# Kernel tuning notes

Measured on AMD Instinct MI355X. Metric: run time of the kernel, lower is better.

Reference implementation:

```python
import jax, jax.numpy as jnp
import numpy as np

B, C, H, W = 32, 512, 64, 64
P = 8            # partition (window) size
HEAD_DIM = 32
N_HEADS = C // HEAD_DIM  # 16
MLP_RATIO = 4
LN_EPS = 1e-5


def _rel_pos_index(p):
    # Swin/MaxViT-style relative position index for a p x p window -> [p*p, p*p]
    coords = np.stack(np.meshgrid(np.arange(p), np.arange(p), indexing='ij'), 0).reshape(2, -1)
    rel = coords[:, :, None] - coords[:, None, :]          # [2, pp, pp]
    rel = rel.transpose(1, 2, 0) + (p - 1)                 # shift to >= 0
    idx = rel[..., 0] * (2 * p - 1) + rel[..., 1]          # [pp, pp]
    return jnp.asarray(idx, jnp.int32)


def setup_inputs() -> dict:
    key = jax.random.key(0)
    ks = jax.random.split(key, 10)
    s = 0.02
    d_ff = MLP_RATIO * C
    inp = {
        'x': jax.random.normal(ks[0], (B, C, H, W), jnp.float32),
        'gamma1': jnp.ones((C,), jnp.float32),
        'beta1': jnp.zeros((C,), jnp.float32),
        'gamma2': jnp.ones((C,), jnp.float32),
        'beta2': jnp.zeros((C,), jnp.float32),
        'qkv_w': jax.random.normal(ks[1], (C, 3 * C), jnp.float32) * s,
        'qkv_b': jnp.zeros((3 * C,), jnp.float32),
        'merge_w': jax.random.normal(ks[2], (C, C), jnp.float32) * s,
        'merge_b': jnp.zeros((C,), jnp.float32),
        'bias_table': jax.random.normal(ks[3], ((2 * P - 1) ** 2, N_HEADS), jnp.float32) * s,
        'w1': jax.random.normal(ks[4], (C, d_ff), jnp.float32) * s,
        'b1': jnp.zeros((d_ff,), jnp.float32),
        'w2': jax.random.normal(ks[5], (d_ff, C), jnp.float32) * s,
        'b2': jnp.zeros((C,), jnp.float32),
        'rel_idx': _rel_pos_index(P),
    }
    return inp


def _layernorm(t, g, b):
    mu = jnp.mean(t, axis=-1, keepdims=True)
    var = jnp.mean(jnp.square(t - mu), axis=-1, keepdims=True)
    return (t - mu) * jax.lax.rsqrt(var + LN_EPS) * g + b


def reference(x, gamma1, beta1, gamma2, beta2, qkv_w, qkv_b, merge_w, merge_b,
              bias_table, w1, b1, w2, b2, rel_idx):
    p, hd, nh = P, HEAD_DIM, N_HEADS
    Bx, Cx, Hx, Wx = x.shape
    hp, wp = Hx // p, Wx // p
    G, PP = hp * wp, p * p

    # --- window partition: [B,C,H,W] -> [B, G, p*p, C] (partition_type='window', no swap)
    xw = x.reshape(Bx, Cx, hp, p, wp, p).transpose(0, 2, 4, 3, 5, 1).reshape(Bx, G, PP, Cx)

    # --- relative-position multi-head attention on norm1(x)
    h = _layernorm(xw, gamma1, beta1)
    qkv = h @ qkv_w + qkv_b                                   # [B,G,PP,3C]
    q, k, v = jnp.split(qkv, 3, axis=-1)
    q = q.reshape(Bx, G, PP, nh, hd) * (hd ** -0.5)
    k = k.reshape(Bx, G, PP, nh, hd)
    v = v.reshape(Bx, G, PP, nh, hd)
    attn = jnp.einsum('bgqhd,bgkhd->bghqk', q, k)             # [B,G,nh,PP,PP]
    bias = bias_table[rel_idx]                                # [PP,PP,nh]
    attn = attn + bias.transpose(2, 0, 1)[None, None]
    attn = jax.nn.softmax(attn, axis=-1)
    o = jnp.einsum('bghqk,bgkhd->bgqhd', attn, v).reshape(Bx, G, PP, Cx)
    xw = xw + (o @ merge_w + merge_b)                          # residual (dropout/SD p=0)

    # --- MLP block on norm2(x)
    h2 = _layernorm(xw, gamma2, beta2)
    m = jax.nn.gelu(h2 @ w1 + b1) @ w2 + b2
    xw = xw + m

    # --- window departition: [B,G,p*p,C] -> [B,C,H,W]
    out = xw.reshape(Bx, hp, wp, p, p, Cx).transpose(0, 5, 1, 3, 2, 4).reshape(Bx, Cx, Hx, Wx)
    return out
```

## Files before the change

### kernel.cpp

```cpp
#include <hip/hip_runtime.h>
#include <stdint.h>

typedef __attribute__((ext_vector_type(8))) short short8;
typedef __attribute__((ext_vector_type(4))) float f32x4;
typedef __attribute__((address_space(3))) void lds_void;
typedef __attribute__((address_space(1))) void gv_void;

static __device__ __forceinline__ float bf2f(unsigned short u) {
    union { uint32_t i; float f; } v; v.i = ((uint32_t)u) << 16; return v.f;
}
static __device__ __forceinline__ unsigned short f2bf(float f) {
    union { float f; uint32_t i; } v; v.f = f;
    uint32_t i = v.i;
    uint32_t r = (i + 0x7fffu + ((i >> 16) & 1u)) >> 16;
    return (unsigned short)r;
}
static __device__ __forceinline__ float fexp(float x) {
    float r;
    asm("v_exp_f32 %0, %1" : "=v"(r) : "v"(x * 1.44269504088896f));
    return r;
}
static __device__ __forceinline__ float frcp(float x) {
    float r;
    asm("v_rcp_f32 %0, %1" : "=v"(r) : "v"(x));
    return r;
}

__global__ void k_detect(const void* __restrict__ g1, int* __restrict__ flag) {
    if (threadIdx.x == 0 && blockIdx.x == 0) {
        const unsigned short* u = (const unsigned short*)g1;
        flag[0] = (u[0] == 0x3F80u) ? 0 : 1;
    }
}

__global__ __launch_bounds__(256) void k_cvt(const void* __restrict__ src,
                                             unsigned short* __restrict__ dst,
                                             int n, const int* __restrict__ flag) {
    int i = blockIdx.x * 256 + threadIdx.x;
    if (i < n) {
        dst[i] = flag[0] ? f2bf(((const float*)src)[i])
                         : ((const unsigned short*)src)[i];
    }
}

__global__ __launch_bounds__(256) void k_transpose(const void* __restrict__ in,
                                                   unsigned short* __restrict__ out,
                                                   int R, int C, const int* __restrict__ flag) {
    __shared__ unsigned short tile[32][33];
    int isf = flag[0];
    int tx = threadIdx.x, ty = threadIdx.y;
    int x = blockIdx.x * 32 + tx;
    int y0 = blockIdx.y * 32;
    for (int j = ty; j < 32; j += 8) {
        size_t idx = (size_t)(y0 + j) * C + x;
        tile[j][tx] = isf ? f2bf(((const float*)in)[idx]) : ((const unsigned short*)in)[idx];
    }
    __syncthreads();
    int x2 = y0 + tx;
    int y20 = blockIdx.x * 32;
    for (int j = ty; j < 32; j += 8)
        out[(size_t)(y20 + j) * R + x2] = tile[tx][j];
}

__global__ __launch_bounds__(256) void k_prep_bias(const void* __restrict__ bias_table,
                                                   const int* __restrict__ rel_idx,
                                                   float* __restrict__ biasp,
                                                   const int* __restrict__ flag) {
    int i = blockIdx.x * 256 + threadIdx.x;
    int isf = flag[0];
    int h = i & 15, qk = i >> 4;
    size_t idx = (size_t)rel_idx[qk] * 16 + h;
    float v = isf ? ((const float*)bias_table)[idx] : bf2f(((const unsigned short*)bias_table)[idx]);
    biasp[h * 4096 + qk] = v;
}

__global__ __launch_bounds__(256) void k_partition_ln(const void* __restrict__ x,
                                                      const unsigned short* __restrict__ g1,
                                                      const unsigned short* __restrict__ b1,
                                                      unsigned short* __restrict__ xw,
                                                      unsigned short* __restrict__ h,
                                                      int b0, const int* __restrict__ flag) {
    __shared__ unsigned short tile[64][512];
    int isf = flag[0];
    int bh = blockIdx.x, bl = bh >> 6, hh = bh & 63;
    int b = b0 + bl;
    int tid = threadIdx.x;
    size_t xoff = (((size_t)b * 512) * 64 + hh) * 64;
    int c0 = tid >> 3, ch = tid & 7;
    if (isf) {
        const float* xb = (const float*)x + xoff;
        for (int k = 0; k < 16; ++k) {
            int c = c0 + k * 32;
            f32x4 v0 = *reinterpret_cast<const f32x4*>(xb + (size_t)c * 4096 + ch * 8);
            f32x4 v1 = *reinterpret_cast<const f32x4*>(xb + (size_t)c * 4096 + ch * 8 + 4);
#pragma unroll
            for (int j = 0; j < 4; ++j) tile[ch * 8 + j][c] = f2bf(v0[j]);
#pragma unroll
            for (int j = 0; j < 4; ++j) tile[ch * 8 + 4 + j][c] = f2bf(v1[j]);
        }
    } else {
        const unsigned short* xb = (const unsigned short*)x + xoff;
        for (int k = 0; k < 16; ++k) {
            int c = c0 + k * 32;
            short8 v = *reinterpret_cast<const short8*>(xb + (size_t)c * 4096 + ch * 8);
#pragma unroll
            for (int j = 0; j < 8; ++j) tile[ch * 8 + j][c] = (unsigned short)v[j];
        }
    }
    __syncthreads();
    int w = tid >> 2, q = tid & 3;
    float s = 0.f, s2 = 0.f;
#pragma unroll 4
    for (int j = 0; j < 128; ++j) {
        int c = q * 128 + ((j + 8 * w) & 127);
        float f = bf2f(tile[w][c]);
        s += f; s2 += f * f;
    }
    s += __shfl_xor(s, 1);  s += __shfl_xor(s, 2);
    s2 += __shfl_xor(s2, 1); s2 += __shfl_xor(s2, 2);
    float mu = s * (1.f / 512.f);
    float rstd = rsqrtf(s2 * (1.f / 512.f) - mu * mu + 1e-5f);
    int t = (bl * 64 + (hh >> 3) * 8 + (w >> 3)) * 64 + (hh & 7) * 8 + (w & 7);
    unsigned short* xr = xw + (size_t)t * 512;
    unsigned short* hr = h + (size_t)t * 512;
    for (int cc = q * 128; cc < q * 128 + 128; cc += 8) {
        short8 raw, hn;
#pragma unroll
        for (int j = 0; j < 8; ++j) {
            unsigned short u = tile[w][cc + j];
            raw[j] = (short)u;
            float f = (bf2f(u) - mu) * rstd * bf2f(g1[cc + j]) + bf2f(b1[cc + j]);
            hn[j] = (short)f2bf(f);
        }
        *reinterpret_cast<short8*>(xr + cc) = raw;
        *reinterpret_cast<short8*>(hr + cc) = hn;
    }
}

__global__ __launch_bounds__(256) void k_ln(const unsigned short* __restrict__ in,
                                            const unsigned short* __restrict__ g,
                                            const unsigned short* __restrict__ b,
                                            unsigned short* __restrict__ out) {
    int wid = threadIdx.x >> 6, lane = threadIdx.x & 63;
    size_t t = (size_t)blockIdx.x * 4 + wid;
    short8 v = *reinterpret_cast<const short8*>(in + t * 512 + lane * 8);
    float f[8], s = 0.f, s2 = 0.f;
#pragma unroll
    for (int j = 0; j < 8; ++j) { f[j] = bf2f((unsigned short)v[j]); s += f[j]; s2 += f[j] * f[j]; }
    for (int m = 1; m < 64; m <<= 1) { s += __shfl_xor(s, m); s2 += __shfl_xor(s2, m); }
    float mu = s * (1.f / 512.f);
    float rstd = rsqrtf(s2 * (1.f / 512.f) - mu * mu + 1e-5f);
    short8 ov;
#pragma unroll
    for (int j = 0; j < 8; ++j)
        ov[j] = (short)f2bf((f[j] - mu) * rstd * bf2f(g[lane * 8 + j]) + bf2f(b[lane * 8 + j]));
    *reinterpret_cast<short8*>(out + t * 512 + lane * 8) = ov;
}

template <int MODE>
__global__ __launch_bounds__(512, 2) void k_gemm3(const unsigned short* __restrict__ A,
                                                  const unsigned short* __restrict__ BT,
                                                  const unsigned short* __restrict__ bias,
                                                  const unsigned short* __restrict__ res,
                                                  unsigned short* __restrict__ out,
                                                  int M, int N, int K) {
    __shared__ unsigned short S[65536];
    const int tid = threadIdx.x, lane = tid & 63, wid = tid >> 6;
    const int mt = blockIdx.x, nt = blockIdx.y;
    const int wr = wid >> 2, wc = wid & 3;
    const int rl = lane & 15, qg = lane >> 4;

    const unsigned short* ApA[2];
    const unsigned short* ApB[2];
#pragma unroll
    for (int h = 0; h < 2; ++h) {
        int row = h * 128 + wid * 16 + (lane >> 2);
        int blk = (lane & 3) ^ ((row >> 1) & 3);
        ApA[h] = A  + (size_t)(mt * 256 + row) * K + blk * 8;
        ApB[h] = BT + (size_t)(nt * 256 + row) * K + blk * 8;
    }

    f32x4 acc[8][4];
#pragma unroll
    for (int mf = 0; mf < 8; ++mf)
#pragma unroll
        for (int nf = 0; nf < 4; ++nf) {
            acc[mf][nf][0] = 0.f; acc[mf][nf][1] = 0.f; acc[mf][nf][2] = 0.f; acc[mf][nf][3] = 0.f;
        }

    const int NT = K >> 5;

    auto stage = [&](int t, int h) {
        int slot = t & 3;
        __builtin_amdgcn_global_load_lds((const gv_void*)(ApA[h] + t * 32),
            (lds_void*)(&S[slot * 16384 + h * 4096 + wid * 512]), 16, 0, 0);
        __builtin_amdgcn_global_load_lds((const gv_void*)(ApB[h] + t * 32),
            (lds_void*)(&S[slot * 16384 + 8192 + h * 4096 + wid * 512]), 16, 0, 0);
    };

    stage(0, 0); stage(0, 1);
    stage(1, 0); stage(1, 1);
    stage(2, 0); stage(2, 1);

    const int xo = ((qg ^ ((rl >> 1) & 3))) * 8;
    const int arow = wr * 128 + rl;
    const int brow = wc * 64 + rl;

    for (int t = 0; t < NT; ++t) {
        const unsigned short* sA = &S[(t & 3) * 16384];
        const unsigned short* sB = sA + 8192;
        if (t + 3 < NT) stage(t + 3, 0);
        if (t + 3 < NT)      { asm volatile("s_waitcnt vmcnt(10)" ::: "memory"); }
        else if (t + 2 < NT) { asm volatile("s_waitcnt vmcnt(8)"  ::: "memory"); }
        else if (t + 1 < NT) { asm volatile("s_waitcnt vmcnt(4)"  ::: "memory"); }
        else                 { asm volatile("s_waitcnt vmcnt(0)"  ::: "memory"); }
        __builtin_amdgcn_s_barrier();
        asm volatile("" ::: "memory");

        short8 bfr[4], af[4];
#pragma unroll
        for (int nf = 0; nf < 4; ++nf)
            bfr[nf] = *reinterpret_cast<const short8*>(&sB[(brow + nf * 16) * 32 + xo]);
#pragma unroll
        for (int mf = 0; mf < 4; ++mf)
            af[mf] = *reinterpret_cast<const short8*>(&sA[(arow + mf * 16) * 32 + xo]);
        if (t + 3 < NT) stage(t + 3, 1);

        __builtin_amdgcn_s_setprio(1);
#pragma unroll
        for (int mf = 0; mf < 4; ++mf)
#pragma unroll
            for (int nf = 0; nf < 4; ++nf)
                acc[mf][nf] = __builtin_amdgcn_mfma_f32_16x16x32_bf16(af[mf], bfr[nf], acc[mf][nf], 0, 0, 0);
        __builtin_amdgcn_s_setprio(0);

        short8 af2[4];
#pragma unroll
        for (int mf = 0; mf < 4; ++mf)
            af2[mf] = *reinterpret_cast<const short8*>(&sA[(arow + 64 + mf * 16) * 32 + xo]);
        __builtin_amdgcn_s_barrier();
        asm volatile("" ::: "memory");
        __builtin_amdgcn_s_setprio(1);
#pragma unroll
        for (int mf = 0; mf < 4; ++mf)
#pragma unroll
            for (int nf = 0; nf < 4; ++nf)
                acc[mf + 4][nf] = __builtin_amdgcn_mfma_f32_16x16x32_bf16(af2[mf], bfr[nf], acc[mf + 4][nf], 0, 0, 0);
        __builtin_amdgcn_s_setprio(0);
        __builtin_amdgcn_s_barrier();
        asm volatile("" ::: "memory");
    }

    const int PST = 272;
    unsigned short* pb = (unsigned short*)S;
    float bz[4];
#pragma unroll
    for (int nf = 0; nf < 4; ++nf) bz[nf] = bf2f(bias[nt * 256 + wc * 64 + nf * 16 + rl]);
    int row_l = tid >> 4, cbl = (tid & 15) * 16;
    int growb = mt * 256 + (row_l >> 4) * 128 + (row_l & 15);
    size_t gcol = (size_t)nt * 256 + cbl;

#pragma unroll
    for (int mf = 0; mf < 8; ++mf) {
        __syncthreads();
#pragma unroll
        for (int nf = 0; nf < 4; ++nf)
#pragma unroll
            for (int r = 0; r < 4; ++r) {
                float v = acc[mf][nf][r] + bz[nf];
                if (MODE == 2) {
                    float z = 0.7978845608f * (v + 0.044715f * v * v * v);
                    float e = fexp(-2.0f * z);
                    v = v * frcp(1.f + e);
                }
                pb[(wr * 16 + qg * 4 + r) * PST + wc * 64 + nf * 16 + rl] = f2bf(v);
            }
        __syncthreads();
        size_t go = (size_t)(growb + mf * 16) * N + gcol;
        short8 o1 = *reinterpret_cast<const short8*>(&pb[row_l * PST + cbl]);
        short8 o2 = *reinterpret_cast<const short8*>(&pb[row_l * PST + cbl + 8]);
        if (MODE == 1) {
            short8 r1 = *reinterpret_cast<const short8*>(&res[go]);
            short8 r2 = *reinterpret_cast<const short8*>(&res[go + 8]);
#pragma unroll
            for (int j = 0; j < 8; ++j) {
                o1[j] = (short)f2bf(bf2f((unsigned short)o1[j]) + bf2f((unsigned short)r1[j]));
                o2[j] = (short)f2bf(bf2f((unsigned short)o2[j]) + bf2f((unsigned short)r2[j]));
            }
        }
        *reinterpret_cast<short8*>(&out[go]) = o1;
        *reinterpret_cast<short8*>(&out[go + 8]) = o2;
    }
}

__global__ __launch_bounds__(64) void k_attn(const unsigned short* __restrict__ qkv,
                                             const float* __restrict__ biasp,
                                             unsigned short* __restrict__ o) {
    __shared__ unsigned short Pl[64][72];
    int blk = blockIdx.x;
    int head = blk & 15, win = blk >> 4;
    size_t T0 = (size_t)win * 64;
    int lane = threadIdx.x;
    int rl = lane & 15, qg = lane >> 4;
    const unsigned short* base = qkv + T0 * 1536;
    int qoff = head * 32, koff = 512 + head * 32, voff = 1024 + head * 32;

    f32x4 s[4][4];
#pragma unroll
    for (int m = 0; m < 4; ++m)
#pragma unroll
        for (int n = 0; n < 4; ++n) { s[m][n][0] = 0.f; s[m][n][1] = 0.f; s[m][n][2] = 0.f; s[m][n][3] = 0.f; }

    short8 aq[4], bk[4];
#pragma unroll
    for (int m = 0; m < 4; ++m)
        aq[m] = *reinterpret_cast<const short8*>(base + (size_t)(16 * m + rl) * 1536 + qoff + qg * 8);
#pragma unroll
    for (int n = 0; n < 4; ++n)
        bk[n] = *reinterpret_cast<const short8*>(base + (size_t)(16 * n + rl) * 1536 + koff + qg * 8);
#pragma unroll
    for (int m = 0; m < 4; ++m)
#pragma unroll
        for (int n = 0; n < 4; ++n)
            s[m][n] = __builtin_amdgcn_mfma_f32_16x16x32_bf16(aq[m], bk[n], s[m][n], 0, 0, 0);

    const float scale = 0.17677669529663687f;
    const float* bh = biasp + head * 4096;
#pragma unroll
    for (int m = 0; m < 4; ++m) {
#pragma unroll
        for (int r = 0; r < 4; ++r) {
            int row = 16 * m + qg * 4 + r;
            float v0 = s[m][0][r] * scale + bh[row * 64 + rl];
            float v1 = s[m][1][r] * scale + bh[row * 64 + 16 + rl];
            float v2 = s[m][2][r] * scale + bh[row * 64 + 32 + rl];
            float v3 = s[m][3][r] * scale + bh[row * 64 + 48 + rl];
            float mx = fmaxf(fmaxf(v0, v1), fmaxf(v2, v3));
            mx = fmaxf(mx, __shfl_xor(mx, 1));
            mx = fmaxf(mx, __shfl_xor(mx, 2));
            mx = fmaxf(mx, __shfl_xor(mx, 4));
            mx = fmaxf(mx, __shfl_xor(mx, 8));
            v0 = fexp(v0 - mx); v1 = fexp(v1 - mx); v2 = fexp(v2 - mx); v3 = fexp(v3 - mx);
            float sm = v0 + v1 + v2 + v3;
            sm += __shfl_xor(sm, 1);
            sm += __shfl_xor(sm, 2);
            sm += __shfl_xor(sm, 4);
            sm += __shfl_xor(sm, 8);
            float inv = frcp(sm);
            Pl[row][rl]      = f2bf(v0 * inv);
            Pl[row][16 + rl] = f2bf(v1 * inv);
            Pl[row][32 + rl] = f2bf(v2 * inv);
            Pl[row][48 + rl] = f2bf(v3 * inv);
        }
    }
    __syncthreads();

    short8 bv[2][2];
#pragma unroll
    for (int ks = 0; ks < 2; ++ks)
#pragma unroll
        for (int n2 = 0; n2 < 2; ++n2) {
            short8 t;
#pragma unroll
            for (int i = 0; i < 8; ++i)
                t[i] = (short)base[(size_t)(32 * ks + qg * 8 + i) * 1536 + voff + n2 * 16 + rl];
            bv[ks][n2] = t;
        }

    f32x4 acc2[4][2];
#pragma unroll
    for (int m = 0; m < 4; ++m)
#pragma unroll
        for (int n2 = 0; n2 < 2; ++n2) { acc2[m][n2][0] = 0.f; acc2[m][n2][1] = 0.f; acc2[m][n2][2] = 0.f; acc2[m][n2][3] = 0.f; }

#pragma unroll
    for (int m = 0; m < 4; ++m) {
        short8 p0 = *reinterpret_cast<const short8*>(&Pl[16 * m + rl][qg * 8]);
        short8 p1 = *reinterpret_cast<const short8*>(&Pl[16 * m + rl][32 + qg * 8]);
#pragma unroll
        for (int n2 = 0; n2 < 2; ++n2) {
            acc2[m][n2] = __builtin_amdgcn_mfma_f32_16x16x32_bf16(p0, bv[0][n2], acc2[m][n2], 0, 0, 0);
            acc2[m][n2] = __builtin_amdgcn_mfma_f32_16x16x32_bf16(p1, bv[1][n2], acc2[m][n2], 0, 0, 0);
        }
    }
#pragma unroll
    for (int m = 0; m < 4; ++m)
#pragma unroll
        for (int n2 = 0; n2 < 2; ++n2)
#pragma unroll
            for (int r = 0; r < 4; ++r) {
                int row = 16 * m + qg * 4 + r;
                o[(T0 + row) * 512 + head * 32 + n2 * 16 + rl] = f2bf(acc2[m][n2][r]);
            }
}

__global__ __launch_bounds__(256) void k_departition(const unsigned short* __restrict__ tok,
                                                     void* __restrict__ xo,
                                                     int b0, const int* __restrict__ flag) {
    __shared__ unsigned short tile[64][512];
    int isf = flag[0];
    int bh = blockIdx.x, bl = bh >> 6, hh = bh & 63;
    int b = b0 + bl;
    int tid = threadIdx.x;
    int Tb = (bl * 64 + (hh >> 3) * 8) * 64 + (hh & 7) * 8;
    for (int k = 0; k < 16; ++k) {
        int flat = k * 256 + tid;
        int w = flat >> 6, ch = flat & 63;
        int t = Tb + (w >> 3) * 64 + (w & 7);
        short8 v = *reinterpret_cast<const short8*>(tok + (size_t)t * 512 + ch * 8);
        *reinterpret_cast<short8*>(&tile[w][ch * 8]) = v;
    }
    __syncthreads();
    size_t xoff = (((size_t)b * 512) * 64 + hh) * 64;
    if (isf) {
        float* xb = (float*)xo + xoff;
        for (int k = 0; k < 16; ++k) {
            int flat = k * 256 + tid;
            int c = flat >> 3, wc = flat & 7;
#pragma unroll
            for (int j = 0; j < 8; ++j)
                xb[(size_t)c * 4096 + wc * 8 + j] = bf2f(tile[wc * 8 + j][c]);
        }
    } else {
        unsigned short* xb = (unsigned short*)xo + xoff;
        for (int k = 0; k < 16; ++k) {
            int flat = k * 256 + tid;
            int c = flat >> 3, wc = flat & 7;
            short8 v;
#pragma unroll
            for (int j = 0; j < 8; ++j) v[j] = (short)tile[wc * 8 + j][c];
            *reinterpret_cast<short8*>(xb + (size_t)c * 4096 + wc * 8) = v;
        }
    }
}

extern "C" void kernel_launch(void* const* d_in, const int* in_sizes, int n_in,
                              void* d_out, int out_size, void* d_ws, size_t ws_size,
                              hipStream_t stream) {
    const void* x          = d_in[0];
    const void* g1         = d_in[1];
    const void* be1        = d_in[2];
    const void* g2         = d_in[3];
    const void* be2        = d_in[4];
    const void* qkv_w      = d_in[5];
    const void* qkv_b      = d_in[6];
    const void* merge_w    = d_in[7];
    const void* merge_b    = d_in[8];
    const void* bias_table = d_in[9];
    const void* w1         = d_in[10];
    const void* b1         = d_in[11];
    const void* w2         = d_in[12];
    const void* b2         = d_in[13];
    const int*  rel_idx    = (const int*)d_in[14];

    const size_t extra = 8u << 20;
    int CB = 4;
    if      (ws_size >= (size_t)131072 * 10240 + extra) CB = 32;
    else if (ws_size >= (size_t)65536  * 10240 + extra) CB = 16;
    else if (ws_size >= (size_t)32768  * 10240 + extra) CB = 8;
    int nch = 32 / CB;
    size_t tok = (size_t)CB * 4096;

    unsigned short* xw_c     = (unsigned short*)d_ws;
    unsigned short* h_c      = xw_c + tok * 512;
    unsigned short* o_c      = h_c + tok * 512;
    unsigned short* qkv_c    = o_c + tok * 512;
    unsigned short* mid_c    = qkv_c + tok * 1536;
    unsigned short* qkv_wT   = mid_c + tok * 2048;
    unsigned short* merge_wT = qkv_wT + 1536 * 512;
    unsigned short* w1T      = merge_wT + 512 * 512;
    unsigned short* w2T      = w1T + 2048 * 512;
    unsigned short* vecs     = w2T + 512 * 2048;
    float*          biasp    = (float*)(vecs + 6656);
    int*            flag     = (int*)(biasp + 65536);

    unsigned short* ng1 = vecs + 0,    *nbe1 = vecs + 512;
    unsigned short* ng2 = vecs + 1024, *nbe2 = vecs + 1536;
    unsigned short* nqb = vecs + 2048, *nmb  = vecs + 3584;
    unsigned short* nb1 = vecs + 4096, *nb2  = vecs + 6144;

    k_detect<<<1, 64, 0, stream>>>(g1, flag);
    k_cvt<<<2, 256, 0, stream>>>(g1, ng1, 512, flag);
    k_cvt<<<2, 256, 0, stream>>>(be1, nbe1, 512, flag);
    k_cvt<<<2, 256, 0, stream>>>(g2, ng2, 512, flag);
    k_cvt<<<2, 256, 0, stream>>>(be2, nbe2, 512, flag);
    k_cvt<<<6, 256, 0, stream>>>(qkv_b, nqb, 1536, flag);
    k_cvt<<<2, 256, 0, stream>>>(merge_b, nmb, 512, flag);
    k_cvt<<<8, 256, 0, stream>>>(b1, nb1, 2048, flag);
    k_cvt<<<2, 256, 0, stream>>>(b2, nb2, 512, flag);
    k_transpose<<<dim3(48, 16), dim3(32, 8), 0, stream>>>(qkv_w, qkv_wT, 512, 1536, flag);
    k_transpose<<<dim3(16, 16), dim3(32, 8), 0, stream>>>(merge_w, merge_wT, 512, 512, flag);
    k_transpose<<<dim3(64, 16), dim3(32, 8), 0, stream>>>(w1, w1T, 512, 2048, flag);
    k_transpose<<<dim3(16, 64), dim3(32, 8), 0, stream>>>(w2, w2T, 2048, 512, flag);
    k_prep_bias<<<256, 256, 0, stream>>>(bias_table, rel_idx, biasp, flag);

    int mtiles = (int)(tok / 256);
    int M = (int)tok;
    for (int c = 0; c < nch; ++c) {
        int b0 = c * CB;
        k_partition_ln<<<CB * 64, 256, 0, stream>>>(x, ng1, nbe1, xw_c, h_c, b0, flag);
        k_gemm3<0><<<dim3(mtiles, 6), 512, 0, stream>>>(h_c, qkv_wT, nqb, nullptr, qkv_c, M, 1536, 512);
        k_attn<<<CB * 1024, 64, 0, stream>>>(qkv_c, biasp, o_c);
        k_gemm3<1><<<dim3(mtiles, 2), 512, 0, stream>>>(o_c, merge_wT, nmb, xw_c, xw_c, M, 512, 512);
        k_ln<<<(int)(tok / 4), 256, 0, stream>>>(xw_c, ng2, nbe2, h_c);
        k_gemm3<2><<<dim3(mtiles, 8), 512, 0, stream>>>(h_c, w1T, nb1, nullptr, mid_c, M, 2048, 512);
        k_gemm3<1><<<dim3(mtiles, 2), 512, 0, stream>>>(mid_c, w2T, nb2, xw_c, qkv_c, M, 512, 2048);
        k_departition<<<CB * 64, 256, 0, stream>>>(qkv_c, d_out, b0, flag);
    }
}
```

Baseline: 1.921 ms.

## Restructure GEMM to double-buffered 64-wide K tiles with swizzled block order

The GEMM mainloop drops the 4-slot, 32-wide K pipeline with split half-tile loads and mid-iteration barriers. It now uses two LDS buffers of 64-wide K tiles with an XOR swizzle, loads the next tile while computing the current one, and syncs once per iteration. Workgroup indices are also remapped so neighbouring blocks share operand tiles in cache. The departition fp32 store becomes two vectorised float4 writes. The tradeoff is a shallower prefetch (only one tile ahead), which may expose more load latency, and the epilogue pad stride changes.

```diff
diff --git a/kernel.cpp b/kernel.cpp
--- a/kernel.cpp
+++ b/kernel.cpp
@@ -158,27 +158,28 @@
 }
 
 template <int MODE>
-__global__ __launch_bounds__(512, 2) void k_gemm3(const unsigned short* __restrict__ A,
+__global__ __launch_bounds__(512, 2) void k_gemm4(const unsigned short* __restrict__ A,
                                                   const unsigned short* __restrict__ BT,
                                                   const unsigned short* __restrict__ bias,
                                                   const unsigned short* __restrict__ res,
                                                   unsigned short* __restrict__ out,
                                                   int M, int N, int K) {
-    __shared__ unsigned short S[65536];
+    __shared__ unsigned short AsS[2][16384];
+    __shared__ unsigned short BsS[2][16384];
     const int tid = threadIdx.x, lane = tid & 63, wid = tid >> 6;
-    const int mt = blockIdx.x, nt = blockIdx.y;
+
+    int nwg = gridDim.x * gridDim.y;
+    int lin = blockIdx.y * gridDim.x + blockIdx.x;
+    int swz = (lin & 7) * (nwg >> 3) + (lin >> 3);
+    int mt = swz % gridDim.x, nt = swz / gridDim.x;
+
     const int wr = wid >> 2, wc = wid & 3;
     const int rl = lane & 15, qg = lane >> 4;
 
-    const unsigned short* ApA[2];
-    const unsigned short* ApB[2];
-#pragma unroll
-    for (int h = 0; h < 2; ++h) {
-        int row = h * 128 + wid * 16 + (lane >> 2);
-        int blk = (lane & 3) ^ ((row >> 1) & 3);
-        ApA[h] = A  + (size_t)(mt * 256 + row) * K + blk * 8;
-        ApB[h] = BT + (size_t)(nt * 256 + row) * K + blk * 8;
-    }
+    const int srow = tid >> 3;
+    const int scb  = (tid & 7) ^ (srow & 7);
+    const unsigned short* Agb = A  + ((size_t)mt * 256 + srow) * K + scb * 8;
+    const unsigned short* Bgb = BT + ((size_t)nt * 256 + srow) * K + scb * 8;
 
     f32x4 acc[8][4];
 #pragma unroll
@@ -188,71 +189,55 @@
             acc[mf][nf][0] = 0.f; acc[mf][nf][1] = 0.f; acc[mf][nf][2] = 0.f; acc[mf][nf][3] = 0.f;
         }
 
-    const int NT = K >> 5;
-
-    auto stage = [&](int t, int h) {
-        int slot = t & 3;
-        __builtin_amdgcn_global_load_lds((const gv_void*)(ApA[h] + t * 32),
-            (lds_void*)(&S[slot * 16384 + h * 4096 + wid * 512]), 16, 0, 0);
-        __builtin_amdgcn_global_load_lds((const gv_void*)(ApB[h] + t * 32),
-            (lds_void*)(&S[slot * 16384 + 8192 + h * 4096 + wid * 512]), 16, 0, 0);
+    const int NT = K >> 6;
+
+    auto stage = [&](int t, int buf) {
+#pragma unroll
+        for (int s = 0; s < 4; ++s) {
+            __builtin_amdgcn_global_load_lds((const gv_void*)(Agb + (size_t)s * 64 * K + t * 64),
+                                             (lds_void*)(&AsS[buf][s * 4096 + tid * 8]), 16, 0, 0);
+            __builtin_amdgcn_global_load_lds((const gv_void*)(Bgb + (size_t)s * 64 * K + t * 64),
+                                             (lds_void*)(&BsS[buf][s * 4096 + tid * 8]), 16, 0, 0);
+        }
     };
 
-    stage(0, 0); stage(0, 1);
-    stage(1, 0); stage(1, 1);
-    stage(2, 0); stage(2, 1);
-
-    const int xo = ((qg ^ ((rl >> 1) & 3))) * 8;
-    const int arow = wr * 128 + rl;
-    const int brow = wc * 64 + rl;
+    stage(0, 0);
+    asm volatile("s_waitcnt vmcnt(0)" ::: "memory");
+    __builtin_amdgcn_s_barrier();
+    asm volatile("" ::: "memory");
+
+    const int arow0 = wr * 128 + rl;
+    const int brow0 = wc * 64 + rl;
+    const int rx = rl & 7;
 
     for (int t = 0; t < NT; ++t) {
-        const unsigned short* sA = &S[(t & 3) * 16384];
-        const unsigned short* sB = sA + 8192;
-        if (t + 3 < NT) stage(t + 3, 0);
-        if (t + 3 < NT)      { asm volatile("s_waitcnt vmcnt(10)" ::: "memory"); }
-        else if (t + 2 < NT) { asm volatile("s_waitcnt vmcnt(8)"  ::: "memory"); }
-        else if (t + 1 < NT) { asm volatile("s_waitcnt vmcnt(4)"  ::: "memory"); }
-        else                 { asm volatile("s_waitcnt vmcnt(0)"  ::: "memory"); }
+        int cur = t & 1;
+        if (t + 1 < NT) stage(t + 1, cur ^ 1);
+#pragma unroll
+        for (int ks = 0; ks < 2; ++ks) {
+            const int kb = ((ks * 4 + qg) ^ rx) * 8;
+            short8 af[8], bfr[4];
+#pragma unroll
+            for (int mf = 0; mf < 8; ++mf)
+                af[mf] = *reinterpret_cast<const short8*>(&AsS[cur][(arow0 + mf * 16) * 64 + kb]);
+#pragma unroll
+            for (int nf = 0; nf < 4; ++nf)
+                bfr[nf] = *reinterpret_cast<const short8*>(&BsS[cur][(brow0 + nf * 16) * 64 + kb]);
+            __builtin_amdgcn_s_setprio(1);
+#pragma unroll
+            for (int mf = 0; mf < 8; ++mf)
+#pragma unroll
+                for (int nf = 0; nf < 4; ++nf)
+                    acc[mf][nf] = __builtin_amdgcn_mfma_f32_16x16x32_bf16(af[mf], bfr[nf], acc[mf][nf], 0, 0, 0);
+            __builtin_amdgcn_s_setprio(0);
+        }
+        asm volatile("s_waitcnt vmcnt(0)" ::: "memory");
         __builtin_amdgcn_s_barrier();
         asm volatile("" ::: "memory");
-
-        short8 bfr[4], af[4];
-#pragma unroll
-        for (int nf = 0; nf < 4; ++nf)
-            bfr[nf] = *reinterpret_cast<const short8*>(&sB[(brow + nf * 16) * 32 + xo]);
-#pragma unroll
-        for (int mf = 0; mf < 4; ++mf)
-            af[mf] = *reinterpret_cast<const short8*>(&sA[(arow + mf * 16) * 32 + xo]);
-        if (t + 3 < NT) stage(t + 3, 1);
-
-        __builtin_amdgcn_s_setprio(1);
-#pragma unroll
-        for (int mf = 0; mf < 4; ++mf)
-#pragma unroll
-            for (int nf = 0; nf < 4; ++nf)
-                acc[mf][nf] = __builtin_amdgcn_mfma_f32_16x16x32_bf16(af[mf], bfr[nf], acc[mf][nf], 0, 0, 0);
-        __builtin_amdgcn_s_setprio(0);
-
-        short8 af2[4];
-#pragma unroll
-        for (int mf = 0; mf < 4; ++mf)
-            af2[mf] = *reinterpret_cast<const short8*>(&sA[(arow + 64 + mf * 16) * 32 + xo]);
-        __builtin_amdgcn_s_barrier();
-        asm volatile("" ::: "memory");
-        __builtin_amdgcn_s_setprio(1);
-#pragma unroll
-        for (int mf = 0; mf < 4; ++mf)
-#pragma unroll
-            for (int nf = 0; nf < 4; ++nf)
-                acc[mf + 4][nf] = __builtin_amdgcn_mfma_f32_16x16x32_bf16(af2[mf], bfr[nf], acc[mf + 4][nf], 0, 0, 0);
-        __builtin_amdgcn_s_setprio(0);
-        __builtin_amdgcn_s_barrier();
-        asm volatile("" ::: "memory");
-    }
-
-    const int PST = 272;
-    unsigned short* pb = (unsigned short*)S;
+    }
+
+    const int PST = 264;
+    unsigned short* pb = (unsigned short*)AsS;
     float bz[4];
 #pragma unroll
     for (int nf = 0; nf < 4; ++nf) bz[nf] = bf2f(bias[nt * 256 + wc * 64 + nf * 16 + rl]);
@@ -417,9 +402,13 @@
         for (int k = 0; k < 16; ++k) {
             int flat = k * 256 + tid;
             int c = flat >> 3, wc = flat & 7;
-#pragma unroll
-            for (int j = 0; j < 8; ++j)
-                xb[(size_t)c * 4096 + wc * 8 + j] = bf2f(tile[wc * 8 + j][c]);
+            f32x4 a, d;
+#pragma unroll
+            for (int j = 0; j < 4; ++j) a[j] = bf2f(tile[wc * 8 + j][c]);
+#pragma unroll
+            for (int j = 0; j < 4; ++j) d[j] = bf2f(tile[wc * 8 + 4 + j][c]);
+            *reinterpret_cast<f32x4*>(xb + (size_t)c * 4096 + wc * 8) = a;
+            *reinterpret_cast<f32x4*>(xb + (size_t)c * 4096 + wc * 8 + 4) = d;
         }
     } else {
         unsigned short* xb = (unsigned short*)xo + xoff;
@@ -499,12 +488,12 @@
     for (int c = 0; c < nch; ++c) {
         int b0 = c * CB;
         k_partition_ln<<<CB * 64, 256, 0, stream>>>(x, ng1, nbe1, xw_c, h_c, b0, flag);
-        k_gemm3<0><<<dim3(mtiles, 6), 512, 0, stream>>>(h_c, qkv_wT, nqb, nullptr, qkv_c, M, 1536, 512);
+        k_gemm4<0><<<dim3(mtiles, 6), 512, 0, stream>>>(h_c, qkv_wT, nqb, nullptr, qkv_c, M, 1536, 512);
         k_attn<<<CB * 1024, 64, 0, stream>>>(qkv_c, biasp, o_c);
-        k_gemm3<1><<<dim3(mtiles, 2), 512, 0, stream>>>(o_c, merge_wT, nmb, xw_c, xw_c, M, 512, 512);
+        k_gemm4<1><<<dim3(mtiles, 2), 512, 0, stream>>>(o_c, merge_wT, nmb, xw_c, xw_c, M, 512, 512);
         k_ln<<<(int)(tok / 4), 256, 0, stream>>>(xw_c, ng2, nbe2, h_c);
-        k_gemm3<2><<<dim3(mtiles, 8), 512, 0, stream>>>(h_c, w1T, nb1, nullptr, mid_c, M, 2048, 512);
-        k_gemm3<1><<<dim3(mtiles, 2), 512, 0, stream>>>(mid_c, w2T, nb2, xw_c, qkv_c, M, 512, 2048);
+        k_gemm4<2><<<dim3(mtiles, 8), 512, 0, stream>>>(h_c, w1T, nb1, nullptr, mid_c, M, 2048, 512);
+        k_gemm4<1><<<dim3(mtiles, 2), 512, 0, stream>>>(mid_c, w2T, nb2, xw_c, qkv_c, M, 512, 2048);
         k_departition<<<CB * 64, 256, 0, stream>>>(qkv_c, d_out, b0, flag);
     }
 }
```

Result: no change. 1.937 ms (+0.8%).
